# Kernel optimization log

Measured on AMD Instinct MI355X. Metric: run time of the kernel, lower is better.

## Reference

```python
import jax, jax.numpy as jnp
import numpy as np
import math as m

Z_BOUNDS = (0.1, 1.0, 10.0)
STEPS = (128, 128)          # coarse samples per log-depth section
N_IMPORTANCE = 128          # fine samples (cfg.renderer.importance_steps)
ALPHA_RW = 1e-4             # cfg.renderer.alpha
INNER = 1.0                 # cfg.scene.inner_bound


def _uniform_z_log(n_rays):
    segs = []
    for i in range(len(STEPS)):
        lo, hi = m.log10(Z_BOUNDS[i]), m.log10(Z_BOUNDS[i + 1])
        segs.append(jnp.linspace(lo, hi - (hi - lo) / STEPS[i], STEPS[i], dtype=jnp.float32))
    zl = jnp.concatenate(segs)
    return jnp.broadcast_to(zl, (n_rays, zl.shape[0]))


def _contract(x):
    # mipnerf360-style contraction (helpers.mipnerf360_scale)
    x = x / INNER
    n = jnp.maximum(jnp.linalg.norm(x, axis=-1, keepdims=True), 1e-8)
    return jnp.where(n <= 1.0, x, (2.0 - 1.0 / n) * x / n)


def _density(s):
    # analytic stand-in for the abstract density() network
    return 25.0 * jnp.exp(-4.0 * jnp.sum(s * s, axis=-1))


def _radiance(s, d):
    # analytic stand-in for the abstract forward(x, d)
    return _density(s), jax.nn.sigmoid(s + 0.1 * d)


def _weights_from_sigma(sig, zl):
    # delta in log-depth space; last delta = 0 (so last alpha = 0), as in source
    delta = jnp.concatenate([zl[:, 1:] - zl[:, :-1], jnp.zeros_like(zl[:, :1])], axis=-1)
    alpha = 1.0 - jnp.exp(-sig * delta)
    alpha_shift = jnp.concatenate([jnp.zeros_like(alpha[:, :1]), alpha[:, :-1]], axis=-1)
    trans = jnp.cumprod(1.0 - alpha_shift, axis=-1)
    return alpha * trans


def _reweight(w):
    S = w.shape[-1]
    wp = jnp.pad(w, ((0, 0), (1, 1)))
    w = 0.5 * (jnp.maximum(wp[:, :-2], wp[:, 1:-1]) + jnp.maximum(wp[:, 1:-1], wp[:, 2:]))
    w = w + ALPHA_RW / S
    scale = jnp.concatenate([jnp.full((s_,), s_ / sum(STEPS), dtype=jnp.float32) for s_ in STEPS])
    w = w * scale
    return w / jnp.sum(w, axis=-1, keepdims=True)


def _sample_pdf(bins, weights, n):
    # inverse-CDF importance sampling (helpers.sample_pdf), deterministic stratified u
    pdf = weights / jnp.sum(weights, axis=-1, keepdims=True)
    cdf = jnp.cumsum(pdf, axis=-1)                     # [N, S]
    u = (jnp.arange(n, dtype=jnp.float32) + 0.5) / n
    u = jnp.broadcast_to(u, (bins.shape[0], n))
    inds = jax.vmap(lambda c, uu: jnp.searchsorted(c, uu, side='right'))(cdf, u)
    S = bins.shape[-1]
    below = jnp.clip(inds - 1, 0, S - 1)
    above = jnp.clip(inds, 0, S - 1)
    tg = lambda a, i: jnp.take_along_axis(a, i, axis=-1)
    c0, c1 = tg(cdf, below), tg(cdf, above)
    b0, b1 = tg(bins, below), tg(bins, above)
    denom = jnp.where(c1 - c0 < 1e-8, 1.0, c1 - c0)
    t = jnp.clip((u - c0) / denom, 0.0, 1.0)
    return b0 + t * (b1 - b0)


def setup_inputs():
    key = jax.random.key(0)
    k1, k2, k3 = jax.random.split(key, 3)
    N = 65536
    rays_o = 0.1 * jax.random.normal(k1, (N, 3), jnp.float32)
    rays_d = jax.random.normal(k2, (N, 3), jnp.float32)
    bg_color = jax.random.uniform(k3, (3,), jnp.float32)
    return {"rays_o": rays_o, "rays_d": rays_d, "bg_color": bg_color}


def reference(rays_o, rays_d, bg_color):
    rays_d = rays_d / jnp.linalg.norm(rays_d, axis=-1, keepdims=True)
    N = rays_o.shape[0]
    # --- efficient_sampling (torch.no_grad in source) ---
    zl = _uniform_z_log(N)                             # [N, 256]
    z = 10.0 ** zl
    xyz = rays_o[:, None, :] + rays_d[:, None, :] * z[..., None]   # [N, 256, 3]
    sig = _density(_contract(xyz))
    w = _weights_from_sigma(sig, zl)
    w_re = _reweight(w)
    zlf = jax.lax.stop_gradient(_sample_pdf(zl, w_re, N_IMPORTANCE))  # [N, 128]
    zf = 10.0 ** zlf
    # --- render ---
    xyzf = rays_o[:, None, :] + rays_d[:, None, :] * zf[..., None]    # [N, 128, 3]
    dirs = jnp.broadcast_to(rays_d[:, None, :], xyzf.shape)
    sigf, rgbf = _radiance(_contract(xyzf), dirs)
    wf = _weights_from_sigma(sigf, zlf)
    image = jnp.einsum('ns,nsc->nc', wf, rgbf)
    invdepth = jnp.sum(wf / zf, axis=-1)
    image = image + (1.0 - jnp.sum(wf, axis=-1))[:, None] * bg_color
    lo, hi = m.log10(Z_BOUNDS[0]), m.log10(Z_BOUNDS[-1])
    z_vals_log_s = (zlf - lo) / (hi - lo)
    return image, wf, z_vals_log_s, invdepth
```

## Files before the change

kernel.cpp:

```cpp
#include <hip/hip_runtime.h>

#define WAVE 64
#define WPB 4
#define BLOCK (WAVE * WPB)
#define SC 256
#define SF 128

__device__ __forceinline__ float fexp2(float x) {
#if __has_builtin(__builtin_amdgcn_exp2f)
    return __builtin_amdgcn_exp2f(x);
#else
    return exp2f(x);
#endif
}
__device__ __forceinline__ float frcp(float x) {
#if __has_builtin(__builtin_amdgcn_rcpf)
    return __builtin_amdgcn_rcpf(x);
#else
    return 1.0f / x;
#endif
}
__device__ __forceinline__ float frsq(float x) {
#if __has_builtin(__builtin_amdgcn_rsqf)
    return __builtin_amdgcn_rsqf(x);
#else
    return rsqrtf(x);
#endif
}

__global__ __launch_bounds__(BLOCK) void nerf_render(
    const float* __restrict__ rays_o, const float* __restrict__ rays_d,
    const float* __restrict__ bgp, float* __restrict__ out, int N) {
    const int wid  = threadIdx.x >> 6;
    const int lane = threadIdx.x & 63;
    const int ray  = blockIdx.x * WPB + wid;
    __shared__ float cdf_s[WPB][SC];
    if (ray >= N) return;

    const float L2_10 = 3.3219280948873623f;
    const float L2_E  = 1.4426950408889634f;
    const float DLT   = 0.0078125f;

    float ox = rays_o[ray * 3 + 0], oy = rays_o[ray * 3 + 1], oz = rays_o[ray * 3 + 2];
    float dx = rays_d[ray * 3 + 0], dy = rays_d[ray * 3 + 1], dz = rays_d[ray * 3 + 2];
    {
        float rn = frsq(dx * dx + dy * dy + dz * dz);
        dx *= rn; dy *= rn; dz *= rn;
    }

    float e[4], w[4];
    float lp = 1.0f;
#pragma unroll
    for (int i = 0; i < 4; i++) {
        int k = (lane << 2) + i;
        float zl = -1.0f + (float)k * DLT;
        float z  = fexp2(zl * L2_10);
        float px = fmaf(dx, z, ox), py = fmaf(dy, z, oy), pz = fmaf(dz, z, oz);
        float nsq = px * px + py * py + pz * pz;
        float ssq;
        if (nsq > 1.0f) { float rn = frsq(nsq); float t2 = 2.0f - rn; ssq = t2 * t2; }
        else            { ssq = nsq; }
        float sig = 25.0f * fexp2(-4.0f * L2_E * ssq);
        float q = (k == SC - 1) ? 0.0f : sig * DLT;
        e[i] = fexp2(-L2_E * q);
        lp *= e[i];
    }
    float ip = lp;
    for (int off = 1; off < 64; off <<= 1) {
        float t = __shfl_up(ip, off, 64);
        if (lane >= off) ip *= t;
    }
    float tin = __shfl_up(ip, 1, 64);
    if (lane == 0) tin = 1.0f;
    {
        float t = tin;
#pragma unroll
        for (int i = 0; i < 4; i++) { w[i] = (1.0f - e[i]) * t; t *= e[i]; }
    }
    float wprev = __shfl_up(w[3], 1, 64);  if (lane == 0)  wprev = 0.0f;
    float wnext = __shfl_down(w[0], 1, 64); if (lane == 63) wnext = 0.0f;
    const float CADD = 1e-4f / 256.0f;
    float wr0 = 0.5f * (fmaxf(wprev, w[0]) + fmaxf(w[0], w[1])) + CADD;
    float wr1 = 0.5f * (fmaxf(w[0], w[1]) + fmaxf(w[1], w[2])) + CADD;
    float wr2 = 0.5f * (fmaxf(w[1], w[2]) + fmaxf(w[2], w[3])) + CADD;
    float wr3 = 0.5f * (fmaxf(w[2], w[3]) + fmaxf(w[3], wnext)) + CADD;
    float s0 = wr0, s1 = s0 + wr1, s2 = s1 + wr2, s3 = s2 + wr3;
    float base = s3;
    for (int off = 1; off < 64; off <<= 1) {
        float t = __shfl_up(base, off, 64);
        if (lane >= off) base += t;
    }
    float tot = __shfl(base, 63, 64);
    float exb = __shfl_up(base, 1, 64);
    if (lane == 0) exb = 0.0f;
    float invT = 1.0f / tot;
    cdf_s[wid][(lane << 2) + 0] = (exb + s0) * invT;
    cdf_s[wid][(lane << 2) + 1] = (exb + s1) * invT;
    cdf_s[wid][(lane << 2) + 2] = (exb + s2) * invT;
    cdf_s[wid][(lane << 2) + 3] = (exb + s3) * invT;
    __syncthreads();
    const float* cdf = cdf_s[wid];

    float zlf[2];
#pragma unroll
    for (int jj = 0; jj < 2; jj++) {
        int j = (lane << 1) + jj;
        float u = ((float)j + 0.5f) * (1.0f / 128.0f);
        int lo = 0, hi = SC;
        while (lo < hi) {
            int mid = (lo + hi) >> 1;
            if (cdf[mid] <= u) lo = mid + 1; else hi = mid;
        }
        int inds  = lo;
        int below = inds - 1; if (below < 0) below = 0;
        int above = inds;     if (above > SC - 1) above = SC - 1;
        float c0 = cdf[below], c1 = cdf[above];
        float b0 = -1.0f + (float)below * DLT;
        float b1 = -1.0f + (float)above * DLT;
        float dnm = c1 - c0;
        dnm = (dnm < 1e-8f) ? 1.0f : dnm;
        float t = (u - c0) / dnm;
        t = t < 0.0f ? 0.0f : (t > 1.0f ? 1.0f : t);
        zlf[jj] = fmaf(t, b1 - b0, b0);
    }

    float zlf2 = __shfl_down(zlf[0], 1, 64);
    float del[2];
    del[0] = zlf[1] - zlf[0];
    del[1] = (lane == 63) ? 0.0f : (zlf2 - zlf[1]);
    float ef[2], rgbv[2][3], invz[2];
    float lpf = 1.0f;
#pragma unroll
    for (int jj = 0; jj < 2; jj++) {
        float zf = fexp2(zlf[jj] * L2_10);
        invz[jj] = frcp(zf);
        float px = fmaf(dx, zf, ox), py = fmaf(dy, zf, oy), pz = fmaf(dz, zf, oz);
        float nsq = px * px + py * py + pz * pz;
        float ssq, fac;
        if (nsq > 1.0f) { float rn = frsq(nsq); float t2 = 2.0f - rn; ssq = t2 * t2; fac = rn * t2; }
        else            { ssq = nsq; fac = 1.0f; }
        float sig = 25.0f * fexp2(-4.0f * L2_E * ssq);
        ef[jj] = fexp2(-L2_E * sig * del[jj]);
        float sx = px * fac, sy = py * fac, sz = pz * fac;
        rgbv[jj][0] = frcp(1.0f + fexp2(-L2_E * fmaf(0.1f, dx, sx)));
        rgbv[jj][1] = frcp(1.0f + fexp2(-L2_E * fmaf(0.1f, dy, sy)));
        rgbv[jj][2] = frcp(1.0f + fexp2(-L2_E * fmaf(0.1f, dz, sz)));
        lpf *= ef[jj];
    }
    float ipf = lpf;
    for (int off = 1; off < 64; off <<= 1) {
        float t = __shfl_up(ipf, off, 64);
        if (lane >= off) ipf *= t;
    }
    float tinf = __shfl_up(ipf, 1, 64);
    if (lane == 0) tinf = 1.0f;
    float wf0 = (1.0f - ef[0]) * tinf;
    float wf1 = (1.0f - ef[1]) * (tinf * ef[0]);

    float ar = wf0 * rgbv[0][0] + wf1 * rgbv[1][0];
    float ag = wf0 * rgbv[0][1] + wf1 * rgbv[1][1];
    float ab = wf0 * rgbv[0][2] + wf1 * rgbv[1][2];
    float aw = wf0 + wf1;
    float ai = wf0 * invz[0] + wf1 * invz[1];
    for (int off = 32; off; off >>= 1) {
        ar += __shfl_xor(ar, off, 64);
        ag += __shfl_xor(ag, off, 64);
        ab += __shfl_xor(ab, off, 64);
        aw += __shfl_xor(aw, off, 64);
        ai += __shfl_xor(ai, off, 64);
    }

    const size_t NN = (size_t)N;
    float* wf_base  = out + 3 * NN;
    float* zvs_base = out + 3 * NN + NN * (size_t)SF;
    float* inv_base = out + 3 * NN + 2 * NN * (size_t)SF;
    size_t col = (size_t)ray * SF + (size_t)(lane << 1);
    *(float2*)(wf_base + col)  = make_float2(wf0, wf1);
    *(float2*)(zvs_base + col) = make_float2((zlf[0] + 1.0f) * 0.5f, (zlf[1] + 1.0f) * 0.5f);
    if (lane == 0) {
        float om = 1.0f - aw;
        out[ray * 3 + 0] = fmaf(om, bgp[0], ar);
        out[ray * 3 + 1] = fmaf(om, bgp[1], ag);
        out[ray * 3 + 2] = fmaf(om, bgp[2], ab);
        inv_base[ray] = ai;
    }
}

extern "C" void kernel_launch(void* const* d_in, const int* in_sizes, int n_in,
                              void* d_out, int out_size, void* d_ws, size_t ws_size,
                              hipStream_t stream) {
    const float* rays_o = (const float*)d_in[0];
    const float* rays_d = (const float*)d_in[1];
    const float* bg     = (const float*)d_in[2];
    float* out = (float*)d_out;
    int N = in_sizes[0] / 3;
    int blocks = (N + WPB - 1) / WPB;
    nerf_render<<<blocks, BLOCK, 0, stream>>>(rays_o, rays_d, bg, out, N);
}
```

Measured before the change: 129.1 us.

## Replace shuffle scans with DPP wave scans and packed float2 math

Prefix products and sums, and the final reductions, now use DPP row-shift and row-broadcast steps instead of ds_bpermute shuffles, with the reduction result taken from lane 63. The block-wide __syncthreads before the CDF search is removed, relying on each wave reading only its own LDS slice. Coarse depths now come from one exp2 times constant ratios rather than four exp2 calls. Arithmetic is packed into float2 vectors, and the binary search is unrolled to a fixed eight steps. This cuts cross-lane communication latency and instruction count, at the cost of depending on wave-local LDS ordering and hardware-specific DPP controls.

```diff
diff --git a/kernel.cpp b/kernel.cpp
--- a/kernel.cpp
+++ b/kernel.cpp
@@ -1,10 +1,11 @@
 #include <hip/hip_runtime.h>
 
-#define WAVE 64
 #define WPB 4
-#define BLOCK (WAVE * WPB)
+#define BLOCK (64 * WPB)
 #define SC 256
 #define SF 128
+
+typedef float v2f __attribute__((ext_vector_type(2)));
 
 __device__ __forceinline__ float fexp2(float x) {
 #if __has_builtin(__builtin_amdgcn_exp2f)
@@ -26,6 +27,40 @@
 #else
     return rsqrtf(x);
 #endif
+}
+
+#define DPPF(oldv, x, ctrl, rmask)                                              \
+    __int_as_float(__builtin_amdgcn_update_dpp(                                 \
+        __float_as_int(oldv), __float_as_int(x), (ctrl), (rmask), 0xf, false))
+
+#define ROW_SHR1   0x111
+#define ROW_SHR2   0x112
+#define ROW_SHR4   0x114
+#define ROW_SHR8   0x118
+#define WAVE_SHR1  0x138
+#define ROW_BC15   0x142
+#define ROW_BC31   0x143
+
+__device__ __forceinline__ float scan_mul_incl(float x) {
+    x *= DPPF(1.0f, x, ROW_SHR1, 0xf);
+    x *= DPPF(1.0f, x, ROW_SHR2, 0xf);
+    x *= DPPF(1.0f, x, ROW_SHR4, 0xf);
+    x *= DPPF(1.0f, x, ROW_SHR8, 0xf);
+    x *= DPPF(1.0f, x, ROW_BC15, 0xa);
+    x *= DPPF(1.0f, x, ROW_BC31, 0xc);
+    return x;
+}
+__device__ __forceinline__ float scan_add_incl(float x) {
+    x += DPPF(0.0f, x, ROW_SHR1, 0xf);
+    x += DPPF(0.0f, x, ROW_SHR2, 0xf);
+    x += DPPF(0.0f, x, ROW_SHR4, 0xf);
+    x += DPPF(0.0f, x, ROW_SHR8, 0xf);
+    x += DPPF(0.0f, x, ROW_BC15, 0xa);
+    x += DPPF(0.0f, x, ROW_BC31, 0xc);
+    return x;
+}
+__device__ __forceinline__ float readlane63(float x) {
+    return __int_as_float(__builtin_amdgcn_readlane(__float_as_int(x), 63));
 }
 
 __global__ __launch_bounds__(BLOCK) void nerf_render(
@@ -40,6 +75,10 @@
     const float L2_10 = 3.3219280948873623f;
     const float L2_E  = 1.4426950408889634f;
     const float DLT   = 0.0078125f;
+    const float C2  = -4.0f * L2_E;
+    const float C1  = -L2_E * 25.0f * DLT;
+    const float C25 = -L2_E * 25.0f;
+    const float CADD = 1e-4f / 256.0f;
 
     float ox = rays_o[ray * 3 + 0], oy = rays_o[ray * 3 + 1], oz = rays_o[ray * 3 + 2];
     float dx = rays_d[ray * 3 + 0], dy = rays_d[ray * 3 + 1], dz = rays_d[ray * 3 + 2];
@@ -48,57 +87,58 @@
         dx *= rn; dy *= rn; dz *= rn;
     }
 
-    float e[4], w[4];
-    float lp = 1.0f;
+    float zl0 = -1.0f + (float)(lane << 2) * DLT;
+    float z0  = fexp2(zl0 * L2_10);
+    v2f zz[2];
+    zz[0].x = z0;                          zz[0].y = z0 * 1.0181517217011025f;
+    zz[1].x = z0 * 1.0366329284377645f;    zz[1].y = z0 * 1.0554494416179205f;
+
+    v2f ee[2];
 #pragma unroll
-    for (int i = 0; i < 4; i++) {
-        int k = (lane << 2) + i;
-        float zl = -1.0f + (float)k * DLT;
-        float z  = fexp2(zl * L2_10);
-        float px = fmaf(dx, z, ox), py = fmaf(dy, z, oy), pz = fmaf(dz, z, oz);
-        float nsq = px * px + py * py + pz * pz;
-        float ssq;
-        if (nsq > 1.0f) { float rn = frsq(nsq); float t2 = 2.0f - rn; ssq = t2 * t2; }
-        else            { ssq = nsq; }
-        float sig = 25.0f * fexp2(-4.0f * L2_E * ssq);
-        float q = (k == SC - 1) ? 0.0f : sig * DLT;
-        e[i] = fexp2(-L2_E * q);
-        lp *= e[i];
-    }
-    float ip = lp;
-    for (int off = 1; off < 64; off <<= 1) {
-        float t = __shfl_up(ip, off, 64);
-        if (lane >= off) ip *= t;
-    }
-    float tin = __shfl_up(ip, 1, 64);
-    if (lane == 0) tin = 1.0f;
-    {
-        float t = tin;
-#pragma unroll
-        for (int i = 0; i < 4; i++) { w[i] = (1.0f - e[i]) * t; t *= e[i]; }
-    }
-    float wprev = __shfl_up(w[3], 1, 64);  if (lane == 0)  wprev = 0.0f;
-    float wnext = __shfl_down(w[0], 1, 64); if (lane == 63) wnext = 0.0f;
-    const float CADD = 1e-4f / 256.0f;
-    float wr0 = 0.5f * (fmaxf(wprev, w[0]) + fmaxf(w[0], w[1])) + CADD;
-    float wr1 = 0.5f * (fmaxf(w[0], w[1]) + fmaxf(w[1], w[2])) + CADD;
-    float wr2 = 0.5f * (fmaxf(w[1], w[2]) + fmaxf(w[2], w[3])) + CADD;
-    float wr3 = 0.5f * (fmaxf(w[2], w[3]) + fmaxf(w[3], wnext)) + CADD;
+    for (int p = 0; p < 2; p++) {
+        v2f z  = zz[p];
+        v2f px = dx * z + ox, py = dy * z + oy, pz = dz * z + oz;
+        v2f nsq = px * px + py * py + pz * pz;
+        v2f rn; rn.x = frsq(nsq.x); rn.y = frsq(nsq.y);
+        v2f t2 = 2.0f - rn;
+        v2f fs = t2 * t2;
+        v2f ssq;
+        ssq.x = nsq.x > 1.0f ? fs.x : nsq.x;
+        ssq.y = nsq.y > 1.0f ? fs.y : nsq.y;
+        v2f sr = C2 * ssq;
+        v2f sg; sg.x = fexp2(sr.x); sg.y = fexp2(sr.y);
+        v2f ea = C1 * sg;
+        ee[p].x = fexp2(ea.x); ee[p].y = fexp2(ea.y);
+    }
+    if (lane == 63) ee[1].y = 1.0f;
+
+    float lp  = (ee[0].x * ee[0].y) * (ee[1].x * ee[1].y);
+    float tp  = scan_mul_incl(lp);
+    float tin = DPPF(1.0f, tp, WAVE_SHR1, 0xf);
+
+    v2f om0 = 1.0f - ee[0], om1 = 1.0f - ee[1];
+    float c1 = ee[0].x, c2 = c1 * ee[0].y, c3 = c2 * ee[1].x;
+    v2f t01; t01.x = tin;      t01.y = tin * c1;
+    v2f t23; t23.x = tin * c2; t23.y = tin * c3;
+    v2f w01 = om0 * t01, w23 = om1 * t23;
+
+    float wprev = DPPF(0.0f, w23.y, WAVE_SHR1, 0xf);
+    float wnext = __shfl_down(w01.x, 1, 64);
+    if (lane == 63) wnext = 0.0f;
+    float m0 = fmaxf(wprev, w01.x), m1 = fmaxf(w01.x, w01.y),
+          m2 = fmaxf(w01.y, w23.x), m3 = fmaxf(w23.x, w23.y),
+          m4 = fmaxf(w23.y, wnext);
+    float wr0 = 0.5f * (m0 + m1) + CADD, wr1 = 0.5f * (m1 + m2) + CADD,
+          wr2 = 0.5f * (m2 + m3) + CADD, wr3 = 0.5f * (m3 + m4) + CADD;
+
     float s0 = wr0, s1 = s0 + wr1, s2 = s1 + wr2, s3 = s2 + wr3;
-    float base = s3;
-    for (int off = 1; off < 64; off <<= 1) {
-        float t = __shfl_up(base, off, 64);
-        if (lane >= off) base += t;
-    }
-    float tot = __shfl(base, 63, 64);
-    float exb = __shfl_up(base, 1, 64);
-    if (lane == 0) exb = 0.0f;
-    float invT = 1.0f / tot;
-    cdf_s[wid][(lane << 2) + 0] = (exb + s0) * invT;
-    cdf_s[wid][(lane << 2) + 1] = (exb + s1) * invT;
-    cdf_s[wid][(lane << 2) + 2] = (exb + s2) * invT;
-    cdf_s[wid][(lane << 2) + 3] = (exb + s3) * invT;
-    __syncthreads();
+    float incl = scan_add_incl(s3);
+    float exb  = DPPF(0.0f, incl, WAVE_SHR1, 0xf);
+    float invT = frcp(readlane63(incl));
+    v2f cdfa; cdfa.x = (exb + s0) * invT; cdfa.y = (exb + s1) * invT;
+    v2f cdfb; cdfb.x = (exb + s2) * invT; cdfb.y = (exb + s3) * invT;
+    *(v2f*)&cdf_s[wid][(lane << 2) + 0] = cdfa;
+    *(v2f*)&cdf_s[wid][(lane << 2) + 2] = cdfb;
     const float* cdf = cdf_s[wid];
 
     float zlf[2];
@@ -107,17 +147,17 @@
         int j = (lane << 1) + jj;
         float u = ((float)j + 0.5f) * (1.0f / 128.0f);
         int lo = 0, hi = SC;
-        while (lo < hi) {
+#pragma unroll
+        for (int it = 0; it < 8; it++) {
             int mid = (lo + hi) >> 1;
             if (cdf[mid] <= u) lo = mid + 1; else hi = mid;
         }
-        int inds  = lo;
-        int below = inds - 1; if (below < 0) below = 0;
-        int above = inds;     if (above > SC - 1) above = SC - 1;
-        float c0 = cdf[below], c1 = cdf[above];
+        int below = lo - 1; if (below < 0) below = 0;
+        int above = lo;     if (above > SC - 1) above = SC - 1;
+        float c0 = cdf[below], c1v = cdf[above];
         float b0 = -1.0f + (float)below * DLT;
         float b1 = -1.0f + (float)above * DLT;
-        float dnm = c1 - c0;
+        float dnm = c1v - c0;
         dnm = (dnm < 1e-8f) ? 1.0f : dnm;
         float t = (u - c0) / dnm;
         t = t < 0.0f ? 0.0f : (t > 1.0f ? 1.0f : t);
@@ -125,59 +165,59 @@
     }
 
     float zlf2 = __shfl_down(zlf[0], 1, 64);
-    float del[2];
-    del[0] = zlf[1] - zlf[0];
-    del[1] = (lane == 63) ? 0.0f : (zlf2 - zlf[1]);
-    float ef[2], rgbv[2][3], invz[2];
-    float lpf = 1.0f;
-#pragma unroll
-    for (int jj = 0; jj < 2; jj++) {
-        float zf = fexp2(zlf[jj] * L2_10);
-        invz[jj] = frcp(zf);
-        float px = fmaf(dx, zf, ox), py = fmaf(dy, zf, oy), pz = fmaf(dz, zf, oz);
-        float nsq = px * px + py * py + pz * pz;
-        float ssq, fac;
-        if (nsq > 1.0f) { float rn = frsq(nsq); float t2 = 2.0f - rn; ssq = t2 * t2; fac = rn * t2; }
-        else            { ssq = nsq; fac = 1.0f; }
-        float sig = 25.0f * fexp2(-4.0f * L2_E * ssq);
-        ef[jj] = fexp2(-L2_E * sig * del[jj]);
-        float sx = px * fac, sy = py * fac, sz = pz * fac;
-        rgbv[jj][0] = frcp(1.0f + fexp2(-L2_E * fmaf(0.1f, dx, sx)));
-        rgbv[jj][1] = frcp(1.0f + fexp2(-L2_E * fmaf(0.1f, dy, sy)));
-        rgbv[jj][2] = frcp(1.0f + fexp2(-L2_E * fmaf(0.1f, dz, sz)));
-        lpf *= ef[jj];
-    }
-    float ipf = lpf;
-    for (int off = 1; off < 64; off <<= 1) {
-        float t = __shfl_up(ipf, off, 64);
-        if (lane >= off) ipf *= t;
-    }
-    float tinf = __shfl_up(ipf, 1, 64);
-    if (lane == 0) tinf = 1.0f;
-    float wf0 = (1.0f - ef[0]) * tinf;
-    float wf1 = (1.0f - ef[1]) * (tinf * ef[0]);
-
-    float ar = wf0 * rgbv[0][0] + wf1 * rgbv[1][0];
-    float ag = wf0 * rgbv[0][1] + wf1 * rgbv[1][1];
-    float ab = wf0 * rgbv[0][2] + wf1 * rgbv[1][2];
-    float aw = wf0 + wf1;
-    float ai = wf0 * invz[0] + wf1 * invz[1];
-    for (int off = 32; off; off >>= 1) {
-        ar += __shfl_xor(ar, off, 64);
-        ag += __shfl_xor(ag, off, 64);
-        ab += __shfl_xor(ab, off, 64);
-        aw += __shfl_xor(aw, off, 64);
-        ai += __shfl_xor(ai, off, 64);
-    }
+    bool  l63  = (lane == 63);
+    v2f del; del.x = zlf[1] - zlf[0]; del.y = l63 ? 0.0f : (zlf2 - zlf[1]);
+    v2f zf;  zf.x = fexp2(zlf[0] * L2_10); zf.y = fexp2(zlf[1] * L2_10);
+    v2f invz; invz.x = frcp(zf.x); invz.y = frcp(zf.y);
+    v2f px = dx * zf + ox, py = dy * zf + oy, pz = dz * zf + oz;
+    v2f nsq = px * px + py * py + pz * pz;
+    v2f rn; rn.x = frsq(nsq.x); rn.y = frsq(nsq.y);
+    v2f t2 = 2.0f - rn;
+    v2f fs = t2 * t2;
+    v2f fc = rn * t2;
+    v2f ssq, fac;
+    ssq.x = nsq.x > 1.0f ? fs.x : nsq.x;  fac.x = nsq.x > 1.0f ? fc.x : 1.0f;
+    ssq.y = nsq.y > 1.0f ? fs.y : nsq.y;  fac.y = nsq.y > 1.0f ? fc.y : 1.0f;
+    v2f sr = C2 * ssq;
+    v2f sg; sg.x = fexp2(sr.x); sg.y = fexp2(sr.y);
+    v2f ea = (C25 * sg) * del;
+    v2f ef; ef.x = fexp2(ea.x); ef.y = fexp2(ea.y);
+
+    v2f sx = px * fac, sy = py * fac, sz = pz * fac;
+    v2f axr = (sx + 0.1f * dx) * (-L2_E);
+    v2f axg = (sy + 0.1f * dy) * (-L2_E);
+    v2f axb = (sz + 0.1f * dz) * (-L2_E);
+    v2f er; er.x = fexp2(axr.x); er.y = fexp2(axr.y);
+    v2f eg; eg.x = fexp2(axg.x); eg.y = fexp2(axg.y);
+    v2f eb; eb.x = fexp2(axb.x); eb.y = fexp2(axb.y);
+    v2f dr = 1.0f + er, dg = 1.0f + eg, db = 1.0f + eb;
+    v2f rv; rv.x = frcp(dr.x); rv.y = frcp(dr.y);
+    v2f gv; gv.x = frcp(dg.x); gv.y = frcp(dg.y);
+    v2f bv; bv.x = frcp(db.x); bv.y = frcp(db.y);
+
+    float lpf  = ef.x * ef.y;
+    float tpf  = scan_mul_incl(lpf);
+    float tinf = DPPF(1.0f, tpf, WAVE_SHR1, 0xf);
+    float wf0 = (1.0f - ef.x) * tinf;
+    float wf1 = (1.0f - ef.y) * (tinf * ef.x);
+    v2f wfv; wfv.x = wf0; wfv.y = wf1;
+
+    v2f pr = wfv * rv, pg = wfv * gv, pb = wfv * bv, pi = wfv * invz;
+    float ar = scan_add_incl(pr.x + pr.y);
+    float ag = scan_add_incl(pg.x + pg.y);
+    float ab = scan_add_incl(pb.x + pb.y);
+    float aw = scan_add_incl(wf0 + wf1);
+    float ai = scan_add_incl(pi.x + pi.y);
 
     const size_t NN = (size_t)N;
     float* wf_base  = out + 3 * NN;
-    float* zvs_base = out + 3 * NN + NN * (size_t)SF;
-    float* inv_base = out + 3 * NN + 2 * NN * (size_t)SF;
+    float* zvs_base = wf_base + NN * (size_t)SF;
+    float* inv_base = zvs_base + NN * (size_t)SF;
     size_t col = (size_t)ray * SF + (size_t)(lane << 1);
-    *(float2*)(wf_base + col)  = make_float2(wf0, wf1);
-    *(float2*)(zvs_base + col) = make_float2((zlf[0] + 1.0f) * 0.5f, (zlf[1] + 1.0f) * 0.5f);
-    if (lane == 0) {
+    *(float2*)(wf_base + col) = make_float2(wf0, wf1);
+    v2f zvs; zvs.x = (zlf[0] + 1.0f) * 0.5f; zvs.y = (zlf[1] + 1.0f) * 0.5f;
+    *(float2*)(zvs_base + col) = make_float2(zvs.x, zvs.y);
+    if (l63) {
         float om = 1.0f - aw;
         out[ray * 3 + 0] = fmaf(om, bgp[0], ar);
         out[ray * 3 + 1] = fmaf(om, bgp[1], ag);
```

Result: faster. 122.8 us (-4.8%).
